# Optimization experiments

Measured on AMD Instinct MI355X. Metric: run time of the kernel, lower is better.

The kernel has to match this reference:

```python
import jax, jax.numpy as jnp
from jax import lax
import numpy as np

MAX_VAL = 255.0
LEVELS = 5
MS_WEIGHTS = np.array([0.0448, 0.2856, 0.3001, 0.2363, 0.1333], dtype=np.float32)


def _gaussian_window(window_size: int, sigma: float) -> jnp.ndarray:
    # 1D gaussian -> outer product -> [1, 1, ws, ws] conv kernel (channel=1 depthwise)
    x = np.arange(window_size, dtype=np.float64)
    g = np.exp(-((x - window_size // 2) ** 2) / (2.0 * sigma ** 2))
    g = (g / g.sum()).astype(np.float32)
    w2d = np.outer(g, g)
    return jnp.asarray(w2d[None, None, :, :])


def _conv_same(x, win, pad):
    return lax.conv_general_dilated(
        x, win, window_strides=(1, 1), padding=[(pad, pad), (pad, pad)],
        dimension_numbers=('NCHW', 'OIHW', 'NCHW'))


def _ssim_level(img1, img2):
    _, _, w, h = img1.shape
    window_size = min(w, h, 11)
    sigma = 1.5 * window_size / 11
    win = _gaussian_window(window_size, sigma)
    pad = window_size // 2

    mu1 = _conv_same(img1, win, pad)
    mu2 = _conv_same(img2, win, pad)
    mu1_sq = mu1 * mu1
    mu2_sq = mu2 * mu2
    mu1_mu2 = mu1 * mu2
    sigma1_sq = _conv_same(img1 * img1, win, pad) - mu1_sq
    sigma2_sq = _conv_same(img2 * img2, win, pad) - mu2_sq
    sigma12 = _conv_same(img1 * img2, win, pad) - mu1_mu2

    C1 = (0.01 * MAX_VAL) ** 2
    C2 = (0.03 * MAX_VAL) ** 2
    V1 = 2.0 * sigma12 + C2
    V2 = sigma1_sq + sigma2_sq + C2
    ssim_map = (2.0 * mu1_mu2 + C1) * V1 / ((mu1_sq + mu2_sq + C1) * V2)
    mcs_map = V1 / V2
    return ssim_map.mean(), mcs_map.mean()


def _avg_pool2(x):
    b, c, h, w = x.shape
    return x.reshape(b, c, h // 2, 2, w // 2, 2).mean(axis=(3, 5))


def _ms_ssim(img1, img2):
    msssim = []
    mcs = []
    for _ in range(LEVELS):
        s, m = _ssim_level(img1, img2)
        msssim.append(s)
        mcs.append(m)
        img1 = _avg_pool2(img1)
        img2 = _avg_pool2(img2)
    weight = jnp.asarray(MS_WEIGHTS)
    mcs = jnp.stack(mcs)
    value = jnp.prod(mcs[:LEVELS - 1] ** weight[:LEVELS - 1]) * msssim[-1] ** weight[LEVELS - 1]
    return jnp.clip(value / 2.0, 0.0, 1.0)


def setup_inputs() -> dict:
    key = jax.random.key(0)
    k1, k2 = jax.random.split(key)
    shape = (16, 1, 512, 512)
    img1 = jax.random.uniform(k1, shape, dtype=jnp.float32)
    img2 = jax.random.uniform(k2, shape, dtype=jnp.float32)
    return {"img1": img1, "img2": img2}


def reference(img1, img2):
    return _ms_ssim(img1, img2)
```

## Files before the change

kernel.cpp:

```cpp
#include <hip/hip_runtime.h>
#include <math.h>


#define WS 11
#define TW 64
#define TH 32
#define SROWS 42
#define HSTRIDE 68

__device__ __forceinline__ void gauss_weights(float* w) {
    float s = 0.f;
#pragma unroll
    for (int j = 0; j < WS; ++j) {
        float d = (float)(j - 5);
        float e = expf(-d * d / 4.5f);
        w[j] = e;
        s += e;
    }
    float inv = 1.f / s;
#pragma unroll
    for (int j = 0; j < WS; ++j) w[j] *= inv;
}

__device__ __forceinline__ void ssim_tile(
    const float* __restrict__ p1, const float* __restrict__ p2,
    int H, int W, int x0, int y0, const float* w,
    float* hS, float* hD, float* hS2, float* hD2,
    float red[2][4], float* __restrict__ partials, int part_idx)
{
    const int tid = threadIdx.x;

#pragma unroll 1
    for (int t = tid; t < SROWS * 16; t += 256) {
        int r = t >> 4, xg = t & 15;
        int gy = y0 - 5 + r;
        int gxb = x0 - 8 + 4 * xg;
        float fs[20], fd[20];
        if (gy >= 0 && gy < H) {
            const float* r1p = p1 + (size_t)gy * W;
            const float* r2p = p2 + (size_t)gy * W;
#pragma unroll
            for (int k = 0; k < 5; ++k) {
                int gx = gxb + 4 * k;
                float4 a = make_float4(0.f, 0.f, 0.f, 0.f);
                float4 c = make_float4(0.f, 0.f, 0.f, 0.f);
                if (gx >= 0 && gx + 3 < W) {
                    a = *(const float4*)(r1p + gx);
                    c = *(const float4*)(r2p + gx);
                } else if (gx + 3 >= 0 && gx < W) {
                    float t1[4] = {0.f, 0.f, 0.f, 0.f};
                    float t2[4] = {0.f, 0.f, 0.f, 0.f};
#pragma unroll
                    for (int u = 0; u < 4; ++u) {
                        int gxx = gx + u;
                        if (gxx >= 0 && gxx < W) { t1[u] = r1p[gxx]; t2[u] = r2p[gxx]; }
                    }
                    a = make_float4(t1[0], t1[1], t1[2], t1[3]);
                    c = make_float4(t2[0], t2[1], t2[2], t2[3]);
                }
                fs[4 * k]     = a.x + c.x;  fd[4 * k]     = a.x - c.x;
                fs[4 * k + 1] = a.y + c.y;  fd[4 * k + 1] = a.y - c.y;
                fs[4 * k + 2] = a.z + c.z;  fd[4 * k + 2] = a.z - c.z;
                fs[4 * k + 3] = a.w + c.w;  fd[4 * k + 3] = a.w - c.w;
            }
        } else {
#pragma unroll
            for (int k = 0; k < 20; ++k) { fs[k] = 0.f; fd[k] = 0.f; }
        }
        float qs[14], qd[14];
#pragma unroll
        for (int k = 0; k < 14; ++k) {
            qs[k] = fs[k + 3] * fs[k + 3];
            qd[k] = fd[k + 3] * fd[k + 3];
        }
        float oS[4], oD[4], oS2[4], oD2[4];
#pragma unroll
        for (int c = 0; c < 4; ++c) {
            float aS = 0.f, aD = 0.f, aS2 = 0.f, aD2 = 0.f;
#pragma unroll
            for (int j = 0; j < WS; ++j) {
                float wj = w[j];
                aS  = fmaf(wj, fs[3 + c + j], aS);
                aD  = fmaf(wj, fd[3 + c + j], aD);
                aS2 = fmaf(wj, qs[c + j], aS2);
                aD2 = fmaf(wj, qd[c + j], aD2);
            }
            oS[c] = aS; oD[c] = aD; oS2[c] = aS2; oD2[c] = aD2;
        }
        int ho = r * HSTRIDE + 4 * xg;
        *(float4*)&hS[ho]  = make_float4(oS[0], oS[1], oS[2], oS[3]);
        *(float4*)&hD[ho]  = make_float4(oD[0], oD[1], oD[2], oD[3]);
        *(float4*)&hS2[ho] = make_float4(oS2[0], oS2[1], oS2[2], oS2[3]);
        *(float4*)&hD2[ho] = make_float4(oD2[0], oD2[1], oD2[2], oD2[3]);
    }
    __syncthreads();

    const int x = tid & 15;
    const int g = tid >> 4;
    float accS[2][4], accD[2][4], accS2[2][4], accD2[2][4];
#pragma unroll
    for (int rr = 0; rr < 2; ++rr)
#pragma unroll
        for (int c = 0; c < 4; ++c) {
            accS[rr][c] = 0.f; accD[rr][c] = 0.f;
            accS2[rr][c] = 0.f; accD2[rr][c] = 0.f;
        }

#pragma unroll
    for (int r = 0; r < 12; ++r) {
        int ho = (2 * g + r) * HSTRIDE + 4 * x;
        float4 vS  = *(const float4*)&hS[ho];
        float4 vD  = *(const float4*)&hD[ho];
        float4 vS2 = *(const float4*)&hS2[ho];
        float4 vD2 = *(const float4*)&hD2[ho];
        float lS[4] = {vS.x, vS.y, vS.z, vS.w};
        float lD[4] = {vD.x, vD.y, vD.z, vD.w};
        float lS2[4] = {vS2.x, vS2.y, vS2.z, vS2.w};
        float lD2[4] = {vD2.x, vD2.y, vD2.z, vD2.w};
        if (r < 11) {
            float wv = w[r];
#pragma unroll
            for (int c = 0; c < 4; ++c) {
                accS[0][c]  = fmaf(wv, lS[c],  accS[0][c]);
                accD[0][c]  = fmaf(wv, lD[c],  accD[0][c]);
                accS2[0][c] = fmaf(wv, lS2[c], accS2[0][c]);
                accD2[0][c] = fmaf(wv, lD2[c], accD2[0][c]);
            }
        }
        if (r >= 1) {
            float wv = w[r - 1];
#pragma unroll
            for (int c = 0; c < 4; ++c) {
                accS[1][c]  = fmaf(wv, lS[c],  accS[1][c]);
                accD[1][c]  = fmaf(wv, lD[c],  accD[1][c]);
                accS2[1][c] = fmaf(wv, lS2[c], accS2[1][c]);
                accD2[1][c] = fmaf(wv, lD2[c], accD2[1][c]);
            }
        }
    }

    const float C1 = 6.5025f;
    const float C2 = 58.5225f;
    const int Hv = min(TH, H - y0);
    const int Wv = min(TW, W - x0);
    float sacc = 0.f, macc = 0.f;
#pragma unroll
    for (int rr = 0; rr < 2; ++rr) {
        int row = 2 * g + rr;
#pragma unroll
        for (int c = 0; c < 4; ++c) {
            float ms = accS[rr][c], md = accD[rr][c];
            float es = accS2[rr][c], ed = accD2[rr][c];
            float ms2 = ms * ms, md2 = md * md;
            float a  = 0.5f * (ms2 - md2);
            float bb = 0.5f * (ms2 + md2);
            float pq = 0.5f * (es - ed);
            float qq = 0.5f * (es + ed);
            float V1 = (pq - a) + C2;
            float V2 = (qq - bb) + C2;
            float num = a + C1;
            float den = bb + C1;
            float inv = 1.0f / (den * V2);
            float sv = num * V1 * inv;
            float mv = V1 * den * inv;
            if (row < Hv && (4 * x + c) < Wv) { sacc += sv; macc += mv; }
        }
    }

#pragma unroll
    for (int o = 32; o > 0; o >>= 1) {
        sacc += __shfl_down(sacc, o);
        macc += __shfl_down(macc, o);
    }
    int wave = tid >> 6, lane = tid & 63;
    if (lane == 0) { red[0][wave] = sacc; red[1][wave] = macc; }
    __syncthreads();
    if (tid == 0) {
        float s = red[0][0] + red[0][1] + red[0][2] + red[0][3];
        float m = red[1][0] + red[1][1] + red[1][2] + red[1][3];
        partials[2 * part_idx] = s;
        partials[2 * part_idx + 1] = m;
    }
}

__global__ __launch_bounds__(256) void ssim_l0_pool_kernel(
    const float* __restrict__ img1, const float* __restrict__ img2,
    float* __restrict__ l1a, float* __restrict__ l1b,
    float* __restrict__ l2a, float* __restrict__ l2b,
    float* __restrict__ l3a, float* __restrict__ l3b,
    float* __restrict__ l4a, float* __restrict__ l4b,
    float* __restrict__ partials)
{
    __shared__ float hS[SROWS * HSTRIDE];
    __shared__ float hD[SROWS * HSTRIDE];
    __shared__ float hS2[SROWS * HSTRIDE];
    __shared__ float hD2[SROWS * HSTRIDE];
    __shared__ float pl1a[16 * 36];
    __shared__ float pl1b[16 * 36];
    __shared__ float red[2][4];

    const int tid = threadIdx.x;
    const int tx = blockIdx.x, ty = blockIdx.y, b = blockIdx.z;
    const int x0 = tx * TW, y0 = ty * TH;
    const float* p1 = img1 + (size_t)b * 512 * 512;
    const float* p2 = img2 + (size_t)b * 512 * 512;

    float w[WS];
    gauss_weights(w);

#pragma unroll 1
    for (int t = tid; t < SROWS * 16; t += 256) {
        int r = t >> 4, xg = t & 15;
        int gy = y0 - 5 + r;
        int gxb = x0 - 8 + 4 * xg;
        float fs[20], fd[20];
        if (gy >= 0 && gy < 512) {
            const float* r1p = p1 + (size_t)gy * 512;
            const float* r2p = p2 + (size_t)gy * 512;
#pragma unroll
            for (int k = 0; k < 5; ++k) {
                int gx = gxb + 4 * k;
                float4 a = make_float4(0.f, 0.f, 0.f, 0.f);
                float4 c = make_float4(0.f, 0.f, 0.f, 0.f);
                if (gx >= 0 && gx + 3 < 512) {
                    a = *(const float4*)(r1p + gx);
                    c = *(const float4*)(r2p + gx);
                } else if (gx + 3 >= 0 && gx < 512) {
                    float t1[4] = {0.f, 0.f, 0.f, 0.f};
                    float t2[4] = {0.f, 0.f, 0.f, 0.f};
#pragma unroll
                    for (int u = 0; u < 4; ++u) {
                        int gxx = gx + u;
                        if (gxx >= 0 && gxx < 512) { t1[u] = r1p[gxx]; t2[u] = r2p[gxx]; }
                    }
                    a = make_float4(t1[0], t1[1], t1[2], t1[3]);
                    c = make_float4(t2[0], t2[1], t2[2], t2[3]);
                }
                fs[4 * k]     = a.x + c.x;  fd[4 * k]     = a.x - c.x;
                fs[4 * k + 1] = a.y + c.y;  fd[4 * k + 1] = a.y - c.y;
                fs[4 * k + 2] = a.z + c.z;  fd[4 * k + 2] = a.z - c.z;
                fs[4 * k + 3] = a.w + c.w;  fd[4 * k + 3] = a.w - c.w;
            }
        } else {
#pragma unroll
            for (int k = 0; k < 20; ++k) { fs[k] = 0.f; fd[k] = 0.f; }
        }
        float qs[14], qd[14];
#pragma unroll
        for (int k = 0; k < 14; ++k) {
            qs[k] = fs[k + 3] * fs[k + 3];
            qd[k] = fd[k + 3] * fd[k + 3];
        }
        float oS[4], oD[4], oS2[4], oD2[4];
#pragma unroll
        for (int c = 0; c < 4; ++c) {
            float aS = 0.f, aD = 0.f, aS2 = 0.f, aD2 = 0.f;
#pragma unroll
            for (int j = 0; j < WS; ++j) {
                float wj = w[j];
                aS  = fmaf(wj, fs[3 + c + j], aS);
                aD  = fmaf(wj, fd[3 + c + j], aD);
                aS2 = fmaf(wj, qs[c + j], aS2);
                aD2 = fmaf(wj, qd[c + j], aD2);
            }
            oS[c] = aS; oD[c] = aD; oS2[c] = aS2; oD2[c] = aD2;
        }
        int ho = r * HSTRIDE + 4 * xg;
        *(float4*)&hS[ho]  = make_float4(oS[0], oS[1], oS[2], oS[3]);
        *(float4*)&hD[ho]  = make_float4(oD[0], oD[1], oD[2], oD[3]);
        *(float4*)&hS2[ho] = make_float4(oS2[0], oS2[1], oS2[2], oS2[3]);
        *(float4*)&hD2[ho] = make_float4(oD2[0], oD2[1], oD2[2], oD2[3]);
    }

    for (int t = tid; t < 512; t += 256) {
        int r = t >> 5, c = t & 31;
        int gy = y0 + 2 * r, gx = x0 + 2 * c;
        const float* a0 = p1 + (size_t)gy * 512 + gx;
        const float* c0 = p2 + (size_t)gy * 512 + gx;
        float2 u0 = *(const float2*)a0;
        float2 u1 = *(const float2*)(a0 + 512);
        float2 t0 = *(const float2*)c0;
        float2 t1 = *(const float2*)(c0 + 512);
        float v1 = 0.25f * ((u0.x + u0.y) + (u1.x + u1.y));
        float v2 = 0.25f * ((t0.x + t0.y) + (t1.x + t1.y));
        size_t o1 = (size_t)b * 256 * 256 + (size_t)(y0 / 2 + r) * 256 + (x0 / 2 + c);
        l1a[o1] = v1;
        l1b[o1] = v2;
        pl1a[r * 36 + c] = v1;
        pl1b[r * 36 + c] = v2;
    }
    __syncthreads();

    if (tid < 64) {
        int lane = tid;
#pragma unroll
        for (int t = lane; t < 128; t += 64) {
            int r = t >> 4, c = t & 15;
            int R = 2 * r, C = 2 * c;
            float v1 = 0.25f * ((pl1a[R * 36 + C] + pl1a[R * 36 + C + 1]) +
                                (pl1a[(R + 1) * 36 + C] + pl1a[(R + 1) * 36 + C + 1]));
            float v2 = 0.25f * ((pl1b[R * 36 + C] + pl1b[R * 36 + C + 1]) +
                                (pl1b[(R + 1) * 36 + C] + pl1b[(R + 1) * 36 + C + 1]));
            size_t o = (size_t)b * 128 * 128 + (size_t)(y0 / 4 + r) * 128 + (x0 / 4 + c);
            l2a[o] = v1;
            l2b[o] = v2;
        }
        if (lane < 32) {
            int r = lane >> 3, c = lane & 7;
            float q1[2][2], q2[2][2];
#pragma unroll
            for (int i = 0; i < 2; ++i)
#pragma unroll
                for (int j = 0; j < 2; ++j) {
                    int R = 4 * r + 2 * i, C = 4 * c + 2 * j;
                    q1[i][j] = 0.25f * ((pl1a[R * 36 + C] + pl1a[R * 36 + C + 1]) +
                                        (pl1a[(R + 1) * 36 + C] + pl1a[(R + 1) * 36 + C + 1]));
                    q2[i][j] = 0.25f * ((pl1b[R * 36 + C] + pl1b[R * 36 + C + 1]) +
                                        (pl1b[(R + 1) * 36 + C] + pl1b[(R + 1) * 36 + C + 1]));
                }
            float v1 = 0.25f * ((q1[0][0] + q1[0][1]) + (q1[1][0] + q1[1][1]));
            float v2 = 0.25f * ((q2[0][0] + q2[0][1]) + (q2[1][0] + q2[1][1]));
            size_t o = (size_t)b * 64 * 64 + (size_t)(y0 / 8 + r) * 64 + (x0 / 8 + c);
            l3a[o] = v1;
            l3b[o] = v2;
        }
        if (lane < 8) {
            int r = lane >> 2, c = lane & 3;
            float p3a[2][2], p3b[2][2];
#pragma unroll
            for (int i3 = 0; i3 < 2; ++i3)
#pragma unroll
                for (int j3 = 0; j3 < 2; ++j3) {
                    float p2a[2][2], p2b[2][2];
#pragma unroll
                    for (int i2 = 0; i2 < 2; ++i2)
#pragma unroll
                        for (int j2 = 0; j2 < 2; ++j2) {
                            int R = 8 * r + 4 * i3 + 2 * i2;
                            int C = 8 * c + 4 * j3 + 2 * j2;
                            p2a[i2][j2] = 0.25f * ((pl1a[R * 36 + C] + pl1a[R * 36 + C + 1]) +
                                                   (pl1a[(R + 1) * 36 + C] + pl1a[(R + 1) * 36 + C + 1]));
                            p2b[i2][j2] = 0.25f * ((pl1b[R * 36 + C] + pl1b[R * 36 + C + 1]) +
                                                   (pl1b[(R + 1) * 36 + C] + pl1b[(R + 1) * 36 + C + 1]));
                        }
                    p3a[i3][j3] = 0.25f * ((p2a[0][0] + p2a[0][1]) + (p2a[1][0] + p2a[1][1]));
                    p3b[i3][j3] = 0.25f * ((p2b[0][0] + p2b[0][1]) + (p2b[1][0] + p2b[1][1]));
                }
            float v1 = 0.25f * ((p3a[0][0] + p3a[0][1]) + (p3a[1][0] + p3a[1][1]));
            float v2 = 0.25f * ((p3b[0][0] + p3b[0][1]) + (p3b[1][0] + p3b[1][1]));
            size_t o = (size_t)b * 32 * 32 + (size_t)(y0 / 16 + r) * 32 + (x0 / 16 + c);
            l4a[o] = v1;
            l4b[o] = v2;
        }
    }

    {
        const int x = tid & 15;
        const int g = tid >> 4;
        float accS[2][4], accD[2][4], accS2[2][4], accD2[2][4];
#pragma unroll
        for (int rr = 0; rr < 2; ++rr)
#pragma unroll
            for (int c = 0; c < 4; ++c) {
                accS[rr][c] = 0.f; accD[rr][c] = 0.f;
                accS2[rr][c] = 0.f; accD2[rr][c] = 0.f;
            }

#pragma unroll
        for (int r = 0; r < 12; ++r) {
            int ho = (2 * g + r) * HSTRIDE + 4 * x;
            float4 vS  = *(const float4*)&hS[ho];
            float4 vD  = *(const float4*)&hD[ho];
            float4 vS2 = *(const float4*)&hS2[ho];
            float4 vD2 = *(const float4*)&hD2[ho];
            float lS[4] = {vS.x, vS.y, vS.z, vS.w};
            float lD[4] = {vD.x, vD.y, vD.z, vD.w};
            float lS2[4] = {vS2.x, vS2.y, vS2.z, vS2.w};
            float lD2[4] = {vD2.x, vD2.y, vD2.z, vD2.w};
            if (r < 11) {
                float wv = w[r];
#pragma unroll
                for (int c = 0; c < 4; ++c) {
                    accS[0][c]  = fmaf(wv, lS[c],  accS[0][c]);
                    accD[0][c]  = fmaf(wv, lD[c],  accD[0][c]);
                    accS2[0][c] = fmaf(wv, lS2[c], accS2[0][c]);
                    accD2[0][c] = fmaf(wv, lD2[c], accD2[0][c]);
                }
            }
            if (r >= 1) {
                float wv = w[r - 1];
#pragma unroll
                for (int c = 0; c < 4; ++c) {
                    accS[1][c]  = fmaf(wv, lS[c],  accS[1][c]);
                    accD[1][c]  = fmaf(wv, lD[c],  accD[1][c]);
                    accS2[1][c] = fmaf(wv, lS2[c], accS2[1][c]);
                    accD2[1][c] = fmaf(wv, lD2[c], accD2[1][c]);
                }
            }
        }

        const float C1 = 6.5025f;
        const float C2 = 58.5225f;
        float sacc = 0.f, macc = 0.f;
#pragma unroll
        for (int rr = 0; rr < 2; ++rr) {
#pragma unroll
            for (int c = 0; c < 4; ++c) {
                float ms = accS[rr][c], md = accD[rr][c];
                float es = accS2[rr][c], ed = accD2[rr][c];
                float ms2 = ms * ms, md2 = md * md;
                float a  = 0.5f * (ms2 - md2);
                float bb = 0.5f * (ms2 + md2);
                float pq = 0.5f * (es - ed);
                float qq = 0.5f * (es + ed);
                float V1 = (pq - a) + C2;
                float V2 = (qq - bb) + C2;
                float num = a + C1;
                float den = bb + C1;
                float inv = 1.0f / (den * V2);
                sacc += num * V1 * inv;
                macc += V1 * den * inv;
            }
        }

#pragma unroll
        for (int o = 32; o > 0; o >>= 1) {
            sacc += __shfl_down(sacc, o);
            macc += __shfl_down(macc, o);
        }
        int wave = tid >> 6, lane = tid & 63;
        if (lane == 0) { red[0][wave] = sacc; red[1][wave] = macc; }
        __syncthreads();
        if (tid == 0) {
            float s = red[0][0] + red[0][1] + red[0][2] + red[0][3];
            float m = red[1][0] + red[1][1] + red[1][2] + red[1][3];
            int linear = ((b * 16 + ty) * 8) + tx;
            partials[2 * linear] = s;
            partials[2 * linear + 1] = m;
        }
    }
}

__global__ __launch_bounds__(256) void ssim_rest_kernel(
    const float* __restrict__ l1a, const float* __restrict__ l1b,
    const float* __restrict__ l2a, const float* __restrict__ l2b,
    const float* __restrict__ l3a, const float* __restrict__ l3b,
    const float* __restrict__ l4a, const float* __restrict__ l4b,
    float* __restrict__ partials)
{
    __shared__ float hS[SROWS * HSTRIDE];
    __shared__ float hD[SROWS * HSTRIDE];
    __shared__ float hS2[SROWS * HSTRIDE];
    __shared__ float hD2[SROWS * HSTRIDE];
    __shared__ float red[2][4];

    const int lin = blockIdx.x;
    int level, base;
    if (lin < 512)      { level = 1; base = 0; }
    else if (lin < 640) { level = 2; base = 512; }
    else if (lin < 672) { level = 3; base = 640; }
    else                { level = 4; base = 672; }
    const int Wt[4]   = {256, 128, 64, 32};
    const int ntxl[4] = {2, 1, 0, 0};
    const int ntyl[4] = {3, 2, 1, 0};
    const int idx = level - 1;
    const int W = Wt[idx], H = W;
    const int li = lin - base;
    const int tx = li & ((1 << ntxl[idx]) - 1);
    const int rem = li >> ntxl[idx];
    const int ty = rem & ((1 << ntyl[idx]) - 1);
    const int b = rem >> ntyl[idx];

    const float* ip1; const float* ip2;
    if (level == 1)      { ip1 = l1a; ip2 = l1b; }
    else if (level == 2) { ip1 = l2a; ip2 = l2b; }
    else if (level == 3) { ip1 = l3a; ip2 = l3b; }
    else                 { ip1 = l4a; ip2 = l4b; }
    const float* p1 = ip1 + (size_t)b * H * W;
    const float* p2 = ip2 + (size_t)b * H * W;

    float w[WS];
    gauss_weights(w);

    ssim_tile(p1, p2, H, W, tx * TW, ty * TH, w, hS, hD, hS2, hD2, red,
              partials, lin);
}

__global__ __launch_bounds__(256) void finalize_kernel(
    const float* __restrict__ partials, float* __restrict__ out)
{
    __shared__ float lvl_s[5], lvl_m[5];
    __shared__ float red[2][4];
    const int nb[5] = {2048, 512, 128, 32, 16};
    const int off[5] = {0, 2048, 2560, 2688, 2720};
    const float npix[5] = {16.f * 512 * 512, 16.f * 256 * 256, 16.f * 128 * 128,
                           16.f * 64 * 64, 16.f * 32 * 32};
    const int tid = threadIdx.x;

    for (int l = 0; l < 5; ++l) {
        float s = 0.f, m = 0.f;
        for (int i = tid; i < nb[l]; i += 256) {
            s += partials[2 * (off[l] + i)];
            m += partials[2 * (off[l] + i) + 1];
        }
#pragma unroll
        for (int o = 32; o > 0; o >>= 1) {
            s += __shfl_down(s, o);
            m += __shfl_down(m, o);
        }
        int wave = tid >> 6, lane = tid & 63;
        if (lane == 0) { red[0][wave] = s; red[1][wave] = m; }
        __syncthreads();
        if (tid == 0) {
            lvl_s[l] = (red[0][0] + red[0][1] + red[0][2] + red[0][3]) / npix[l];
            lvl_m[l] = (red[1][0] + red[1][1] + red[1][2] + red[1][3]) / npix[l];
        }
        __syncthreads();
    }

    if (tid == 0) {
        const float w[5] = {0.0448f, 0.2856f, 0.3001f, 0.2363f, 0.1333f};
        float v = powf(lvl_m[0], w[0]) * powf(lvl_m[1], w[1]) * powf(lvl_m[2], w[2]) *
                  powf(lvl_m[3], w[3]) * powf(lvl_s[4], w[4]);
        v *= 0.5f;
        v = fminf(fmaxf(v, 0.f), 1.f);
        out[0] = v;
    }
}

extern "C" void kernel_launch(void* const* d_in, const int* in_sizes, int n_in,
                              void* d_out, int out_size, void* d_ws, size_t ws_size,
                              hipStream_t stream) {
    const float* img1 = (const float*)d_in[0];
    const float* img2 = (const float*)d_in[1];
    float* out = (float*)d_out;

    const int B = 16;

    float* wsf = (float*)d_ws;
    float* partials = wsf;
    float* p = wsf + 5472;
    float* l1a = p; p += (size_t)B * 256 * 256;
    float* l1b = p; p += (size_t)B * 256 * 256;
    float* l2a = p; p += (size_t)B * 128 * 128;
    float* l2b = p; p += (size_t)B * 128 * 128;
    float* l3a = p; p += (size_t)B * 64 * 64;
    float* l3b = p; p += (size_t)B * 64 * 64;
    float* l4a = p; p += (size_t)B * 32 * 32;
    float* l4b = p; p += (size_t)B * 32 * 32;

    dim3 block(256);

    ssim_l0_pool_kernel<<<dim3(8, 16, B), block, 0, stream>>>(
        img1, img2, l1a, l1b, l2a, l2b, l3a, l3b, l4a, l4b, partials);

    ssim_rest_kernel<<<dim3(688), block, 0, stream>>>(
        l1a, l1b, l2a, l2b, l3a, l3b, l4a, l4b, partials + 2 * 2048);

    finalize_kernel<<<1, block, 0, stream>>>(partials, out);
}
```

Baseline: 124.6 us.

## Store horizontal-pass SSIM intermediates as packed half2 in LDS, add interior fast path

The horizontal Gaussian pass now writes its four outputs (sum, diff and their squares) as two packed __half2 arrays instead of four float arrays. This halves LDS footprint and LDS traffic and raises occupancy, with launch bounds now asking for 4 blocks per CU. An interior-tile fast path skips the per-element bounds checks, and the strided loop is unrolled into fixed task calls. The risk is precision loss: second-moment values near 255^2 sums (squares up to ~260k) can exceed fp16 range (max 65504) and lose accuracy in the variance subtraction.

```diff
diff --git a/kernel.cpp b/kernel.cpp
--- a/kernel.cpp
+++ b/kernel.cpp
@@ -1,4 +1,5 @@
 #include <hip/hip_runtime.h>
+#include <hip/hip_fp16.h>
 #include <math.h>
 
 
@@ -22,79 +23,90 @@
     for (int j = 0; j < WS; ++j) w[j] *= inv;
 }
 
-__device__ __forceinline__ void ssim_tile(
-    const float* __restrict__ p1, const float* __restrict__ p2,
-    int H, int W, int x0, int y0, const float* w,
-    float* hS, float* hD, float* hS2, float* hD2,
+__device__ __forceinline__ void h_task(
+    int t, const float* __restrict__ p1, const float* __restrict__ p2,
+    int W, int x0, int y0, bool interior, const float* w,
+    __half2* __restrict__ hSD, __half2* __restrict__ hQ)
+{
+    int r = t >> 4, xg = t & 15;
+    int gy = y0 - 5 + r;
+    int gxb = x0 - 8 + 4 * xg;
+    float fs[20], fd[20];
+    if (interior) {
+        const float* r1p = p1 + (size_t)gy * W + gxb;
+        const float* r2p = p2 + (size_t)gy * W + gxb;
+#pragma unroll
+        for (int k = 0; k < 5; ++k) {
+            float4 a = *(const float4*)(r1p + 4 * k);
+            float4 c = *(const float4*)(r2p + 4 * k);
+            fs[4 * k]     = a.x + c.x;  fd[4 * k]     = a.x - c.x;
+            fs[4 * k + 1] = a.y + c.y;  fd[4 * k + 1] = a.y - c.y;
+            fs[4 * k + 2] = a.z + c.z;  fd[4 * k + 2] = a.z - c.z;
+            fs[4 * k + 3] = a.w + c.w;  fd[4 * k + 3] = a.w - c.w;
+        }
+    } else if (gy >= 0 && gy < W) {
+        const float* r1p = p1 + (size_t)gy * W;
+        const float* r2p = p2 + (size_t)gy * W;
+#pragma unroll
+        for (int k = 0; k < 5; ++k) {
+            int gx = gxb + 4 * k;
+            float4 a = make_float4(0.f, 0.f, 0.f, 0.f);
+            float4 c = make_float4(0.f, 0.f, 0.f, 0.f);
+            if (gx >= 0 && gx + 3 < W) {
+                a = *(const float4*)(r1p + gx);
+                c = *(const float4*)(r2p + gx);
+            } else if (gx + 3 >= 0 && gx < W) {
+                float t1[4] = {0.f, 0.f, 0.f, 0.f};
+                float t2[4] = {0.f, 0.f, 0.f, 0.f};
+#pragma unroll
+                for (int u = 0; u < 4; ++u) {
+                    int gxx = gx + u;
+                    if (gxx >= 0 && gxx < W) { t1[u] = r1p[gxx]; t2[u] = r2p[gxx]; }
+                }
+                a = make_float4(t1[0], t1[1], t1[2], t1[3]);
+                c = make_float4(t2[0], t2[1], t2[2], t2[3]);
+            }
+            fs[4 * k]     = a.x + c.x;  fd[4 * k]     = a.x - c.x;
+            fs[4 * k + 1] = a.y + c.y;  fd[4 * k + 1] = a.y - c.y;
+            fs[4 * k + 2] = a.z + c.z;  fd[4 * k + 2] = a.z - c.z;
+            fs[4 * k + 3] = a.w + c.w;  fd[4 * k + 3] = a.w - c.w;
+        }
+    } else {
+#pragma unroll
+        for (int k = 0; k < 20; ++k) { fs[k] = 0.f; fd[k] = 0.f; }
+    }
+    float qs[14], qd[14];
+#pragma unroll
+    for (int k = 0; k < 14; ++k) {
+        qs[k] = fs[k + 3] * fs[k + 3];
+        qd[k] = fd[k + 3] * fd[k + 3];
+    }
+    __half2 outSD[4], outQ[4];
+#pragma unroll
+    for (int c = 0; c < 4; ++c) {
+        float aS = 0.f, aD = 0.f, aS2 = 0.f, aD2 = 0.f;
+#pragma unroll
+        for (int j = 0; j < WS; ++j) {
+            float wj = w[j];
+            aS  = fmaf(wj, fs[3 + c + j], aS);
+            aD  = fmaf(wj, fd[3 + c + j], aD);
+            aS2 = fmaf(wj, qs[c + j], aS2);
+            aD2 = fmaf(wj, qd[c + j], aD2);
+        }
+        outSD[c] = __float22half2_rn(make_float2(aS, aD));
+        outQ[c]  = __float22half2_rn(make_float2(aS2, aD2));
+    }
+    int ho = r * HSTRIDE + 4 * xg;
+    *(float4*)&hSD[ho] = *(const float4*)outSD;
+    *(float4*)&hQ[ho]  = *(const float4*)outQ;
+}
+
+__device__ __forceinline__ void v_phase(
+    int W, int x0, int y0, const float* w,
+    const __half2* __restrict__ hSD, const __half2* __restrict__ hQ,
     float red[2][4], float* __restrict__ partials, int part_idx)
 {
     const int tid = threadIdx.x;
-
-#pragma unroll 1
-    for (int t = tid; t < SROWS * 16; t += 256) {
-        int r = t >> 4, xg = t & 15;
-        int gy = y0 - 5 + r;
-        int gxb = x0 - 8 + 4 * xg;
-        float fs[20], fd[20];
-        if (gy >= 0 && gy < H) {
-            const float* r1p = p1 + (size_t)gy * W;
-            const float* r2p = p2 + (size_t)gy * W;
-#pragma unroll
-            for (int k = 0; k < 5; ++k) {
-                int gx = gxb + 4 * k;
-                float4 a = make_float4(0.f, 0.f, 0.f, 0.f);
-                float4 c = make_float4(0.f, 0.f, 0.f, 0.f);
-                if (gx >= 0 && gx + 3 < W) {
-                    a = *(const float4*)(r1p + gx);
-                    c = *(const float4*)(r2p + gx);
-                } else if (gx + 3 >= 0 && gx < W) {
-                    float t1[4] = {0.f, 0.f, 0.f, 0.f};
-                    float t2[4] = {0.f, 0.f, 0.f, 0.f};
-#pragma unroll
-                    for (int u = 0; u < 4; ++u) {
-                        int gxx = gx + u;
-                        if (gxx >= 0 && gxx < W) { t1[u] = r1p[gxx]; t2[u] = r2p[gxx]; }
-                    }
-                    a = make_float4(t1[0], t1[1], t1[2], t1[3]);
-                    c = make_float4(t2[0], t2[1], t2[2], t2[3]);
-                }
-                fs[4 * k]     = a.x + c.x;  fd[4 * k]     = a.x - c.x;
-                fs[4 * k + 1] = a.y + c.y;  fd[4 * k + 1] = a.y - c.y;
-                fs[4 * k + 2] = a.z + c.z;  fd[4 * k + 2] = a.z - c.z;
-                fs[4 * k + 3] = a.w + c.w;  fd[4 * k + 3] = a.w - c.w;
-            }
-        } else {
-#pragma unroll
-            for (int k = 0; k < 20; ++k) { fs[k] = 0.f; fd[k] = 0.f; }
-        }
-        float qs[14], qd[14];
-#pragma unroll
-        for (int k = 0; k < 14; ++k) {
-            qs[k] = fs[k + 3] * fs[k + 3];
-            qd[k] = fd[k + 3] * fd[k + 3];
-        }
-        float oS[4], oD[4], oS2[4], oD2[4];
-#pragma unroll
-        for (int c = 0; c < 4; ++c) {
-            float aS = 0.f, aD = 0.f, aS2 = 0.f, aD2 = 0.f;
-#pragma unroll
-            for (int j = 0; j < WS; ++j) {
-                float wj = w[j];
-                aS  = fmaf(wj, fs[3 + c + j], aS);
-                aD  = fmaf(wj, fd[3 + c + j], aD);
-                aS2 = fmaf(wj, qs[c + j], aS2);
-                aD2 = fmaf(wj, qd[c + j], aD2);
-            }
-            oS[c] = aS; oD[c] = aD; oS2[c] = aS2; oD2[c] = aD2;
-        }
-        int ho = r * HSTRIDE + 4 * xg;
-        *(float4*)&hS[ho]  = make_float4(oS[0], oS[1], oS[2], oS[3]);
-        *(float4*)&hD[ho]  = make_float4(oD[0], oD[1], oD[2], oD[3]);
-        *(float4*)&hS2[ho] = make_float4(oS2[0], oS2[1], oS2[2], oS2[3]);
-        *(float4*)&hD2[ho] = make_float4(oD2[0], oD2[1], oD2[2], oD2[3]);
-    }
-    __syncthreads();
-
     const int x = tid & 15;
     const int g = tid >> 4;
     float accS[2][4], accD[2][4], accS2[2][4], accD2[2][4];
@@ -109,14 +121,17 @@
 #pragma unroll
     for (int r = 0; r < 12; ++r) {
         int ho = (2 * g + r) * HSTRIDE + 4 * x;
-        float4 vS  = *(const float4*)&hS[ho];
-        float4 vD  = *(const float4*)&hD[ho];
-        float4 vS2 = *(const float4*)&hS2[ho];
-        float4 vD2 = *(const float4*)&hD2[ho];
-        float lS[4] = {vS.x, vS.y, vS.z, vS.w};
-        float lD[4] = {vD.x, vD.y, vD.z, vD.w};
-        float lS2[4] = {vS2.x, vS2.y, vS2.z, vS2.w};
-        float lD2[4] = {vD2.x, vD2.y, vD2.z, vD2.w};
+        float4 rawSD = *(const float4*)&hSD[ho];
+        float4 rawQ  = *(const float4*)&hQ[ho];
+        const __half2* hpSD = (const __half2*)&rawSD;
+        const __half2* hpQ  = (const __half2*)&rawQ;
+        float lS[4], lD[4], lS2[4], lD2[4];
+#pragma unroll
+        for (int c = 0; c < 4; ++c) {
+            float2 sd = __half22float2(hpSD[c]);
+            float2 q  = __half22float2(hpQ[c]);
+            lS[c] = sd.x; lD[c] = sd.y; lS2[c] = q.x; lD2[c] = q.y;
+        }
         if (r < 11) {
             float wv = w[r];
 #pragma unroll
@@ -141,7 +156,7 @@
 
     const float C1 = 6.5025f;
     const float C2 = 58.5225f;
-    const int Hv = min(TH, H - y0);
+    const int Hv = min(TH, W - y0);
     const int Wv = min(TW, W - x0);
     float sacc = 0.f, macc = 0.f;
 #pragma unroll
@@ -183,7 +198,7 @@
     }
 }
 
-__global__ __launch_bounds__(256) void ssim_l0_pool_kernel(
+__global__ __launch_bounds__(256, 4) void ssim_l0_pool_kernel(
     const float* __restrict__ img1, const float* __restrict__ img2,
     float* __restrict__ l1a, float* __restrict__ l1b,
     float* __restrict__ l2a, float* __restrict__ l2b,
@@ -191,10 +206,8 @@
     float* __restrict__ l4a, float* __restrict__ l4b,
     float* __restrict__ partials)
 {
-    __shared__ float hS[SROWS * HSTRIDE];
-    __shared__ float hD[SROWS * HSTRIDE];
-    __shared__ float hS2[SROWS * HSTRIDE];
-    __shared__ float hD2[SROWS * HSTRIDE];
+    __shared__ __half2 hSD[SROWS * HSTRIDE];
+    __shared__ __half2 hQ[SROWS * HSTRIDE];
     __shared__ float pl1a[16 * 36];
     __shared__ float pl1b[16 * 36];
     __shared__ float red[2][4];
@@ -208,71 +221,16 @@
     float w[WS];
     gauss_weights(w);
 
-#pragma unroll 1
-    for (int t = tid; t < SROWS * 16; t += 256) {
-        int r = t >> 4, xg = t & 15;
-        int gy = y0 - 5 + r;
-        int gxb = x0 - 8 + 4 * xg;
-        float fs[20], fd[20];
-        if (gy >= 0 && gy < 512) {
-            const float* r1p = p1 + (size_t)gy * 512;
-            const float* r2p = p2 + (size_t)gy * 512;
-#pragma unroll
-            for (int k = 0; k < 5; ++k) {
-                int gx = gxb + 4 * k;
-                float4 a = make_float4(0.f, 0.f, 0.f, 0.f);
-                float4 c = make_float4(0.f, 0.f, 0.f, 0.f);
-                if (gx >= 0 && gx + 3 < 512) {
-                    a = *(const float4*)(r1p + gx);
-                    c = *(const float4*)(r2p + gx);
-                } else if (gx + 3 >= 0 && gx < 512) {
-                    float t1[4] = {0.f, 0.f, 0.f, 0.f};
-                    float t2[4] = {0.f, 0.f, 0.f, 0.f};
-#pragma unroll
-                    for (int u = 0; u < 4; ++u) {
-                        int gxx = gx + u;
-                        if (gxx >= 0 && gxx < 512) { t1[u] = r1p[gxx]; t2[u] = r2p[gxx]; }
-                    }
-                    a = make_float4(t1[0], t1[1], t1[2], t1[3]);
-                    c = make_float4(t2[0], t2[1], t2[2], t2[3]);
-                }
-                fs[4 * k]     = a.x + c.x;  fd[4 * k]     = a.x - c.x;
-                fs[4 * k + 1] = a.y + c.y;  fd[4 * k + 1] = a.y - c.y;
-                fs[4 * k + 2] = a.z + c.z;  fd[4 * k + 2] = a.z - c.z;
-                fs[4 * k + 3] = a.w + c.w;  fd[4 * k + 3] = a.w - c.w;
-            }
-        } else {
-#pragma unroll
-            for (int k = 0; k < 20; ++k) { fs[k] = 0.f; fd[k] = 0.f; }
-        }
-        float qs[14], qd[14];
-#pragma unroll
-        for (int k = 0; k < 14; ++k) {
-            qs[k] = fs[k + 3] * fs[k + 3];
-            qd[k] = fd[k + 3] * fd[k + 3];
-        }
-        float oS[4], oD[4], oS2[4], oD2[4];
-#pragma unroll
-        for (int c = 0; c < 4; ++c) {
-            float aS = 0.f, aD = 0.f, aS2 = 0.f, aD2 = 0.f;
-#pragma unroll
-            for (int j = 0; j < WS; ++j) {
-                float wj = w[j];
-                aS  = fmaf(wj, fs[3 + c + j], aS);
-                aD  = fmaf(wj, fd[3 + c + j], aD);
-                aS2 = fmaf(wj, qs[c + j], aS2);
-                aD2 = fmaf(wj, qd[c + j], aD2);
-            }
-            oS[c] = aS; oD[c] = aD; oS2[c] = aS2; oD2[c] = aD2;
-        }
-        int ho = r * HSTRIDE + 4 * xg;
-        *(float4*)&hS[ho]  = make_float4(oS[0], oS[1], oS[2], oS[3]);
-        *(float4*)&hD[ho]  = make_float4(oD[0], oD[1], oD[2], oD[3]);
-        *(float4*)&hS2[ho] = make_float4(oS2[0], oS2[1], oS2[2], oS2[3]);
-        *(float4*)&hD2[ho] = make_float4(oD2[0], oD2[1], oD2[2], oD2[3]);
-    }
-
-    for (int t = tid; t < 512; t += 256) {
+    const bool interior = (x0 >= 8) && (x0 <= 512 - 72) && (y0 >= 5) && (y0 <= 512 - 37);
+
+    h_task(tid,       p1, p2, 512, x0, y0, interior, w, hSD, hQ);
+    h_task(tid + 256, p1, p2, 512, x0, y0, interior, w, hSD, hQ);
+    if (tid < 160)
+        h_task(tid + 512, p1, p2, 512, x0, y0, interior, w, hSD, hQ);
+
+#pragma unroll
+    for (int q = 0; q < 2; ++q) {
+        int t = tid + q * 256;
         int r = t >> 5, c = t & 31;
         int gy = y0 + 2 * r, gx = x0 + 2 * c;
         const float* a0 = p1 + (size_t)gy * 512 + gx;
@@ -354,106 +312,22 @@
         }
     }
 
-    {
-        const int x = tid & 15;
-        const int g = tid >> 4;
-        float accS[2][4], accD[2][4], accS2[2][4], accD2[2][4];
-#pragma unroll
-        for (int rr = 0; rr < 2; ++rr)
-#pragma unroll
-            for (int c = 0; c < 4; ++c) {
-                accS[rr][c] = 0.f; accD[rr][c] = 0.f;
-                accS2[rr][c] = 0.f; accD2[rr][c] = 0.f;
-            }
-
-#pragma unroll
-        for (int r = 0; r < 12; ++r) {
-            int ho = (2 * g + r) * HSTRIDE + 4 * x;
-            float4 vS  = *(const float4*)&hS[ho];
-            float4 vD  = *(const float4*)&hD[ho];
-            float4 vS2 = *(const float4*)&hS2[ho];
-            float4 vD2 = *(const float4*)&hD2[ho];
-            float lS[4] = {vS.x, vS.y, vS.z, vS.w};
-            float lD[4] = {vD.x, vD.y, vD.z, vD.w};
-            float lS2[4] = {vS2.x, vS2.y, vS2.z, vS2.w};
-            float lD2[4] = {vD2.x, vD2.y, vD2.z, vD2.w};
-            if (r < 11) {
-                float wv = w[r];
-#pragma unroll
-                for (int c = 0; c < 4; ++c) {
-                    accS[0][c]  = fmaf(wv, lS[c],  accS[0][c]);
-                    accD[0][c]  = fmaf(wv, lD[c],  accD[0][c]);
-                    accS2[0][c] = fmaf(wv, lS2[c], accS2[0][c]);
-                    accD2[0][c] = fmaf(wv, lD2[c], accD2[0][c]);
-                }
-            }
-            if (r >= 1) {
-                float wv = w[r - 1];
-#pragma unroll
-                for (int c = 0; c < 4; ++c) {
-                    accS[1][c]  = fmaf(wv, lS[c],  accS[1][c]);
-                    accD[1][c]  = fmaf(wv, lD[c],  accD[1][c]);
-                    accS2[1][c] = fmaf(wv, lS2[c], accS2[1][c]);
-                    accD2[1][c] = fmaf(wv, lD2[c], accD2[1][c]);
-                }
-            }
-        }
-
-        const float C1 = 6.5025f;
-        const float C2 = 58.5225f;
-        float sacc = 0.f, macc = 0.f;
-#pragma unroll
-        for (int rr = 0; rr < 2; ++rr) {
-#pragma unroll
-            for (int c = 0; c < 4; ++c) {
-                float ms = accS[rr][c], md = accD[rr][c];
-                float es = accS2[rr][c], ed = accD2[rr][c];
-                float ms2 = ms * ms, md2 = md * md;
-                float a  = 0.5f * (ms2 - md2);
-                float bb = 0.5f * (ms2 + md2);
-                float pq = 0.5f * (es - ed);
-                float qq = 0.5f * (es + ed);
-                float V1 = (pq - a) + C2;
-                float V2 = (qq - bb) + C2;
-                float num = a + C1;
-                float den = bb + C1;
-                float inv = 1.0f / (den * V2);
-                sacc += num * V1 * inv;
-                macc += V1 * den * inv;
-            }
-        }
-
-#pragma unroll
-        for (int o = 32; o > 0; o >>= 1) {
-            sacc += __shfl_down(sacc, o);
-            macc += __shfl_down(macc, o);
-        }
-        int wave = tid >> 6, lane = tid & 63;
-        if (lane == 0) { red[0][wave] = sacc; red[1][wave] = macc; }
-        __syncthreads();
-        if (tid == 0) {
-            float s = red[0][0] + red[0][1] + red[0][2] + red[0][3];
-            float m = red[1][0] + red[1][1] + red[1][2] + red[1][3];
-            int linear = ((b * 16 + ty) * 8) + tx;
-            partials[2 * linear] = s;
-            partials[2 * linear + 1] = m;
-        }
-    }
-}
-
-__global__ __launch_bounds__(256) void ssim_rest_kernel(
+    int part_idx = ((b * 16 + ty) * 8) + tx;
+    v_phase(512, x0, y0, w, hSD, hQ, red, partials, part_idx);
+}
+
+__global__ __launch_bounds__(256, 4) void ssim_rest_kernel(
     const float* __restrict__ l1a, const float* __restrict__ l1b,
     const float* __restrict__ l2a, const float* __restrict__ l2b,
     const float* __restrict__ l3a, const float* __restrict__ l3b,
     const float* __restrict__ l4a, const float* __restrict__ l4b,
     float* __restrict__ partials)
 {
-    __shared__ float hS[SROWS * HSTRIDE];
-    __shared__ float hD[SROWS * HSTRIDE];
-    __shared__ float hS2[SROWS * HSTRIDE];
-    __shared__ float hD2[SROWS * HSTRIDE];
+    __shared__ __half2 hSD[SROWS * HSTRIDE];
+    __shared__ __half2 hQ[SROWS * HSTRIDE];
     __shared__ float red[2][4];
 
+    const int tid = threadIdx.x;
     const int lin = blockIdx.x;
     int level, base;
     if (lin < 512)      { level = 1; base = 0; }
@@ -464,7 +338,7 @@
     const int ntxl[4] = {2, 1, 0, 0};
     const int ntyl[4] = {3, 2, 1, 0};
     const int idx = level - 1;
-    const int W = Wt[idx], H = W;
+    const int W = Wt[idx];
     const int li = lin - base;
     const int tx = li & ((1 << ntxl[idx]) - 1);
     const int rem = li >> ntxl[idx];
@@ -476,14 +350,23 @@
     else if (level == 2) { ip1 = l2a; ip2 = l2b; }
     else if (level == 3) { ip1 = l3a; ip2 = l3b; }
     else                 { ip1 = l4a; ip2 = l4b; }
-    const float* p1 = ip1 + (size_t)b * H * W;
-    const float* p2 = ip2 + (size_t)b * H * W;
+    const float* p1 = ip1 + (size_t)b * W * W;
+    const float* p2 = ip2 + (size_t)b * W * W;
+
+    const int x0 = tx * TW, y0 = ty * TH;
 
     float w[WS];
     gauss_weights(w);
 
-    ssim_tile(p1, p2, H, W, tx * TW, ty * TH, w, hS, hD, hS2, hD2, red,
-              partials, lin);
+    const bool interior = (x0 >= 8) && (x0 <= W - 72) && (y0 >= 5) && (y0 <= W - 37);
+
+    h_task(tid,       p1, p2, W, x0, y0, interior, w, hSD, hQ);
+    h_task(tid + 256, p1, p2, W, x0, y0, interior, w, hSD, hQ);
+    if (tid < 160)
+        h_task(tid + 512, p1, p2, W, x0, y0, interior, w, hSD, hQ);
+    __syncthreads();
+
+    v_phase(W, x0, y0, w, hSD, hQ, red, partials, lin);
 }
 
 __global__ __launch_bounds__(256) void finalize_kernel(
```

Result: slower. 254.7 us (+104.5%).
